# Kernel tuning notes

Measured on AMD Instinct MI355X. Metric: run time of the kernel, lower is better.

## Reference

```python
import jax, jax.numpy as jnp
import numpy as np

B, S, D = 2, 2048, 1024
H = 16
HD = D // H


def setup_inputs() -> dict:
    key = jax.random.key(0)
    k = jax.random.split(key, 5)
    s = 0.02
    return {
        "x": jax.random.normal(k[0], (B, S, D), jnp.float32),
        "w_qkv": jax.random.normal(k[1], (3 * D, D), jnp.float32) * s,
        "b_qkv": jax.random.normal(k[2], (3 * D,), jnp.float32) * s,
        "w_out": jax.random.normal(k[3], (D, D), jnp.float32) * s,
        "b_out": jax.random.normal(k[4], (D,), jnp.float32) * s,
    }


def reference(x, w_qkv, b_qkv, w_out, b_out):
    b, s, d = x.shape
    h, hd = H, HD
    scale = hd ** -0.5
    # QKV projection: [B,S,3D] -> [3,B,H,S,hd]
    qkv = x @ w_qkv.T + b_qkv
    qkv = qkv.reshape(b, s, 3, h, hd).transpose(2, 0, 3, 1, 4)
    q, k, v = qkv[0], qkv[1], qkv[2]
    # Attention scores [B,H,S,S]
    scores = jnp.einsum("bhqd,bhkd->bhqk", q, k) * scale
    attn = jax.nn.softmax(scores, axis=-1)
    # Attend and merge heads
    attended = jnp.einsum("bhqk,bhkd->bqhd", attn, v).reshape(b, s, d)
    return attended @ w_out.T + b_out
```

## Files before the change

kernel.cpp:

```cpp
#include <hip/hip_runtime.h>
#include <hip/hip_bf16.h>

typedef __hip_bfloat16 bf16;
typedef __attribute__((ext_vector_type(8))) short short8;
typedef __attribute__((ext_vector_type(8))) __bf16 bf16x8;
typedef __attribute__((ext_vector_type(4))) float f32x4;
typedef __attribute__((ext_vector_type(16))) float f32x16;
typedef __attribute__((ext_vector_type(4))) unsigned int u32x4;
typedef __attribute__((ext_vector_type(2))) unsigned int u32x2;

#define MFMA16(a, b, c)                                                        \
  __builtin_amdgcn_mfma_f32_16x16x32_bf16(__builtin_bit_cast(bf16x8, (a)),     \
                                          __builtin_bit_cast(bf16x8, (b)),     \
                                          (c), 0, 0, 0)
#define MFMA32(a, b, c)                                                        \
  __builtin_amdgcn_mfma_f32_32x32x16_bf16(__builtin_bit_cast(bf16x8, (a)),     \
                                          __builtin_bit_cast(bf16x8, (b)),     \
                                          (c), 0, 0, 0)

#define GLD16(gsrc, ldst)                                                      \
  __builtin_amdgcn_global_load_lds(                                            \
      (const __attribute__((address_space(1))) void*)(gsrc),                   \
      (__attribute__((address_space(3))) void*)(ldst), 16, 0, 0)

__device__ inline short f2bfs(float f) {
  return __builtin_bit_cast(short, __float2bfloat16(f));
}
__device__ inline unsigned pk2(float lo, float hi) {
  unsigned a = (unsigned short)__builtin_bit_cast(short, __float2bfloat16(lo));
  unsigned b = (unsigned short)__builtin_bit_cast(short, __float2bfloat16(hi));
  return a | (b << 16);
}

template <typename T> __device__ inline short8 ld8bf(const T* p);
template <> __device__ inline short8 ld8bf<bf16>(const bf16* p) {
  return *(const short8*)p;
}
template <> __device__ inline short8 ld8bf<float>(const float* p) {
  f32x4 a = *(const f32x4*)p;
  f32x4 b = *(const f32x4*)(p + 4);
  short8 r;
  r[0] = f2bfs(a[0]); r[1] = f2bfs(a[1]); r[2] = f2bfs(a[2]); r[3] = f2bfs(a[3]);
  r[4] = f2bfs(b[0]); r[5] = f2bfs(b[1]); r[6] = f2bfs(b[2]); r[7] = f2bfs(b[3]);
  return r;
}

template <typename OT> __device__ inline void st1(OT* p, float v);
template <> __device__ inline void st1<bf16>(bf16* p, float v) {
  *p = __float2bfloat16(v);
}
template <> __device__ inline void st1<float>(float* p, float v) { *p = v; }

__device__ inline unsigned int funnel16(unsigned int hi, unsigned int lo) {
  return (unsigned int)(((((unsigned long long)hi) << 32) | lo) >> 16);
}
__device__ inline short8 rotl8(short8 v, int r) {
  u32x4 W = __builtin_bit_cast(u32x4, v);
  u32x4 T, U, F;
  int wr = r >> 1;
  T[0] = (wr & 1) ? W[1] : W[0];
  T[1] = (wr & 1) ? W[2] : W[1];
  T[2] = (wr & 1) ? W[3] : W[2];
  T[3] = (wr & 1) ? W[0] : W[3];
  U[0] = (wr & 2) ? T[2] : T[0];
  U[1] = (wr & 2) ? T[3] : T[1];
  U[2] = (wr & 2) ? T[0] : T[2];
  U[3] = (wr & 2) ? T[1] : T[3];
  F[0] = (r & 1) ? funnel16(U[1], U[0]) : U[0];
  F[1] = (r & 1) ? funnel16(U[2], U[1]) : U[1];
  F[2] = (r & 1) ? funnel16(U[3], U[2]) : U[2];
  F[3] = (r & 1) ? funnel16(U[0], U[3]) : U[3];
  return __builtin_bit_cast(short8, F);
}

__global__ __launch_bounds__(256) void cvt3(
    const float* __restrict__ s0, bf16* __restrict__ d0, int n0,
    const float* __restrict__ s1, bf16* __restrict__ d1, int n1,
    const float* __restrict__ s2, bf16* __restrict__ d2, int n2) {
  int i = (blockIdx.x * 256 + threadIdx.x) * 8;
  if (i < n0) {
    *(short8*)&d0[i] = ld8bf(s0 + i);
  } else if ((i -= n0) < n1) {
    *(short8*)&d1[i] = ld8bf(s1 + i);
  } else if ((i -= n1) < n2) {
    *(short8*)&d2[i] = ld8bf(s2 + i);
  }
}

template <typename OT>
__global__ __launch_bounds__(256, 2) void gemm_lds_bias(
    const bf16* __restrict__ A, const bf16* __restrict__ B,
    const float* __restrict__ bias, OT* __restrict__ C, int M, int N, int K) {
  __shared__ bf16 As[128][64];
  __shared__ bf16 Bs[128][64];

  const int tid = threadIdx.x;
  const int w = tid >> 6, l = tid & 63;
  const int wr = w >> 1, wc = w & 1;
  const int m0 = blockIdx.y * 128, n0 = blockIdx.x * 128;

  f32x4 acc[4][4] = {};

  const int srow = l >> 3;
  const int scol = (l & 7) * 8;

  for (int kt = 0; kt < K; kt += 64) {
#pragma unroll
    for (int j = 0; j < 4; ++j) {
      int chunk = w * 4 + j;
      int row = chunk * 8 + srow;
      GLD16(A + (size_t)(m0 + row) * K + kt + scol, &As[0][0] + chunk * 512);
      GLD16(B + (size_t)(n0 + row) * K + kt + scol, &Bs[0][0] + chunk * 512);
    }
    __syncthreads();

#pragma unroll
    for (int kk = 0; kk < 2; ++kk) {
      short8 af[4], bfv[4];
#pragma unroll
      for (int i = 0; i < 4; ++i) {
        af[i]  = *(const short8*)&As[wr * 64 + i * 16 + (l & 15)]
                                   [kk * 32 + (l >> 4) * 8];
        bfv[i] = *(const short8*)&Bs[wc * 64 + i * 16 + (l & 15)]
                                   [kk * 32 + (l >> 4) * 8];
      }
#pragma unroll
      for (int i = 0; i < 4; ++i)
#pragma unroll
        for (int jn = 0; jn < 4; ++jn)
          acc[i][jn] = MFMA16(af[i], bfv[jn], acc[i][jn]);
    }
    __syncthreads();
  }

#pragma unroll
  for (int i = 0; i < 4; ++i) {
    int rbase = m0 + wr * 64 + i * 16 + (l >> 4) * 4;
#pragma unroll
    for (int jn = 0; jn < 4; ++jn) {
      int col = n0 + wc * 64 + jn * 16 + (l & 15);
      float bv = bias[col];
#pragma unroll
      for (int r = 0; r < 4; ++r)
        st1(&C[(size_t)(rbase + r) * N + col], acc[i][jn][r] + bv);
    }
  }
}

template <typename AT, typename OT>
__global__ __launch_bounds__(256, 2) void gemm_bt_bias(
    const AT* __restrict__ A, const float* __restrict__ B,
    const float* __restrict__ bias, OT* __restrict__ C, int M, int N, int K) {
  __shared__ bf16 As[128][64];
  __shared__ bf16 Bs[128][64];

  const int tid = threadIdx.x;
  const int w = tid >> 6, l = tid & 63;
  const int wr = w >> 1, wc = w & 1;
  const int m0 = blockIdx.y * 128, n0 = blockIdx.x * 128;

  f32x4 acc[4][4] = {};

  const int srow = tid >> 3;
  const int scol = (tid & 7) * 8;

  for (int kt = 0; kt < K; kt += 64) {
    short8 aReg[4], bReg[4];
#pragma unroll
    for (int p = 0; p < 4; ++p) {
      int row = p * 32 + srow;
      aReg[p] = ld8bf(A + (size_t)(m0 + row) * K + kt + scol);
      bReg[p] = ld8bf(B + (size_t)(n0 + row) * K + kt + scol);
    }
    __syncthreads();
#pragma unroll
    for (int p = 0; p < 4; ++p) {
      int row = p * 32 + srow;
      *(short8*)&As[row][scol] = aReg[p];
      *(short8*)&Bs[row][scol] = bReg[p];
    }
    __syncthreads();

#pragma unroll
    for (int kk = 0; kk < 2; ++kk) {
      short8 af[4], bfv[4];
#pragma unroll
      for (int i = 0; i < 4; ++i) {
        af[i]  = *(const short8*)&As[wr * 64 + i * 16 + (l & 15)]
                                   [kk * 32 + (l >> 4) * 8];
        bfv[i] = *(const short8*)&Bs[wc * 64 + i * 16 + (l & 15)]
                                   [kk * 32 + (l >> 4) * 8];
      }
#pragma unroll
      for (int i = 0; i < 4; ++i)
#pragma unroll
        for (int jn = 0; jn < 4; ++jn)
          acc[i][jn] = MFMA16(af[i], bfv[jn], acc[i][jn]);
    }
  }

#pragma unroll
  for (int i = 0; i < 4; ++i) {
    int rbase = m0 + wr * 64 + i * 16 + (l >> 4) * 4;
#pragma unroll
    for (int jn = 0; jn < 4; ++jn) {
      int col = n0 + wc * 64 + jn * 16 + (l & 15);
      float bv = bias[col];
#pragma unroll
      for (int r = 0; r < 4; ++r)
        st1(&C[(size_t)(rbase + r) * N + col], acc[i][jn][r] + bv);
    }
  }
}

__global__ __launch_bounds__(256, 2) void attn_fwd(
    const bf16* __restrict__ qkv, bf16* __restrict__ attended) {
  const int S = 2048, D3 = 3072, D = 1024;
  const int flat = blockIdx.y * 16 + blockIdx.x;
  const int n = (flat & 7) * 64 + (flat >> 3);
  const int qt = n & 15, bh = n >> 4;
  const int b = bh >> 4, h = bh & 15;
  const int tid = threadIdx.x, w = tid >> 6, l = tid & 63;
  const int lo5 = l & 31, hi = l >> 5;

  __shared__ bf16 Klds[128][72];
  __shared__ bf16 Vt[64][136];

  const int q0w = qt * 128 + w * 32;

  short8 qf[4];
  {
    size_t qrow = (size_t)(b * S + q0w + lo5) * D3 + h * 64;
#pragma unroll
    for (int ks = 0; ks < 4; ++ks)
      qf[ks] = *(const short8*)&qkv[qrow + ks * 16 + hi * 8];
  }

  float m_raw = -1e30f, l_i = 0.f;
  f32x16 o0 = {}, o1 = {};

  const float Cs = 0.125f * 1.44269504088896340736f;

  const int srow = tid >> 2;
  const int scq = tid & 3;
  const size_t gb0 = (size_t)(b * S + srow) * D3 + h * 64 + scq * 16;
  const size_t HSTEP = (size_t)64 * D3;

  short8 k0, k1, k2, k3, v0, v1, v2, v3;
  {
    const bf16* g = qkv + gb0;
    k0 = *(const short8*)&g[1024];
    k1 = *(const short8*)&g[1024 + 8];
    v0 = *(const short8*)&g[2048];
    v1 = *(const short8*)&g[2048 + 8];
    const bf16* g2 = g + HSTEP;
    k2 = *(const short8*)&g2[1024];
    k3 = *(const short8*)&g2[1024 + 8];
    v2 = *(const short8*)&g2[2048];
    v3 = *(const short8*)&g2[2048 + 8];
  }

#define PACKP(G, SV)                                                           \
  {                                                                            \
    _Pragma("unroll") for (int tq = 0; tq < 4; ++tq) {                         \
      po[G][tq][0] = pk2((SV)[4 * tq], (SV)[4 * tq + 1]);                      \
      po[G][tq][1] = pk2((SV)[4 * tq + 2], (SV)[4 * tq + 3]);                  \
    }                                                                          \
  }

  for (int t = 0; t < 16; ++t) {
    __syncthreads();
    *(short8*)&Klds[srow][scq * 16] = k0;
    *(short8*)&Klds[srow][scq * 16 + 8] = k1;
    *(short8*)&Klds[64 + srow][scq * 16] = k2;
    *(short8*)&Klds[64 + srow][scq * 16 + 8] = k3;
#pragma unroll
    for (int g = 0; g < 2; ++g) {
      int sI = scq * 2 + g;
      short8 ua = rotl8(g ? v1 : v0, sI);
      short8 ub = rotl8(g ? v3 : v2, sI);
#pragma unroll
      for (int j = 0; j < 8; ++j) {
        int jj = (j + sI) & 7;
        *(short*)&Vt[sI * 8 + jj][srow] = (short)ua[j];
        *(short*)&Vt[sI * 8 + jj][64 + srow] = (short)ub[j];
      }
    }
    __syncthreads();

    if (t + 1 < 16) {
      const bf16* g = qkv + gb0 + (size_t)(t + 1) * 2 * HSTEP;
      k0 = *(const short8*)&g[1024];
      k1 = *(const short8*)&g[1024 + 8];
      k2 = *(const short8*)&g[HSTEP + 1024];
      k3 = *(const short8*)&g[HSTEP + 1024 + 8];
    }

    f32x16 s0 = {}, s1 = {}, s2 = {}, s3 = {};
    __builtin_amdgcn_s_setprio(1);
#pragma unroll
    for (int ks = 0; ks < 4; ++ks) {
      short8 km0 = *(const short8*)&Klds[lo5][ks * 16 + hi * 8];
      short8 km1 = *(const short8*)&Klds[32 + lo5][ks * 16 + hi * 8];
      short8 km2 = *(const short8*)&Klds[64 + lo5][ks * 16 + hi * 8];
      short8 km3 = *(const short8*)&Klds[96 + lo5][ks * 16 + hi * 8];
      s0 = MFMA32(km0, qf[ks], s0);
      s1 = MFMA32(km1, qf[ks], s1);
      s2 = MFMA32(km2, qf[ks], s2);
      s3 = MFMA32(km3, qf[ks], s3);
    }
    __builtin_amdgcn_s_setprio(0);

    if (t + 1 < 16) {
      const bf16* g = qkv + gb0 + (size_t)(t + 1) * 2 * HSTEP;
      v0 = *(const short8*)&g[2048];
      v1 = *(const short8*)&g[2048 + 8];
      v2 = *(const short8*)&g[HSTEP + 2048];
      v3 = *(const short8*)&g[HSTEP + 2048 + 8];
    }

    f32x16 tm;
#pragma unroll
    for (int r = 0; r < 16; ++r)
      tm[r] = fmaxf(fmaxf(s0[r], s1[r]), fmaxf(s2[r], s3[r]));
#pragma unroll
    for (int st = 8; st > 0; st >>= 1)
#pragma unroll
      for (int r = 0; r < st; ++r) tm[r] = fmaxf(tm[r], tm[r + st]);
    float mx = fmaxf(tm[0], __shfl_xor(tm[0], 32));

    bool deferred = __all((mx - m_raw) * Cs <= 8.0f);
    float mn, alpha;
    if (deferred) {
      mn = m_raw;
      alpha = 1.0f;
    } else {
      mn = fmaxf(m_raw, mx);
      alpha = __builtin_amdgcn_exp2f((m_raw - mn) * Cs);
      m_raw = mn;
    }
    float pc = mn * Cs;

#pragma unroll
    for (int r = 0; r < 16; ++r) {
      s0[r] = __builtin_amdgcn_exp2f(__builtin_fmaf(s0[r], Cs, -pc));
      s1[r] = __builtin_amdgcn_exp2f(__builtin_fmaf(s1[r], Cs, -pc));
      s2[r] = __builtin_amdgcn_exp2f(__builtin_fmaf(s2[r], Cs, -pc));
      s3[r] = __builtin_amdgcn_exp2f(__builtin_fmaf(s3[r], Cs, -pc));
    }
    f32x16 ts;
#pragma unroll
    for (int r = 0; r < 16; ++r)
      ts[r] = (s0[r] + s1[r]) + (s2[r] + s3[r]);
#pragma unroll
    for (int st = 8; st > 0; st >>= 1)
#pragma unroll
      for (int r = 0; r < st; ++r) ts[r] += ts[r + st];
    float sf = ts[0] + __shfl_xor(ts[0], 32);
    if (deferred) {
      l_i += sf;
    } else {
      l_i = l_i * alpha + sf;
      o0 *= alpha;
      o1 *= alpha;
    }

    unsigned po[4][4][2];
    PACKP(0, s0) PACKP(1, s1) PACKP(2, s2) PACKP(3, s3)
    unsigned pr[4][2][2];
#pragma unroll
    for (int g = 0; g < 4; ++g)
#pragma unroll
      for (int p = 0; p < 2; ++p)
#pragma unroll
        for (int hf = 0; hf < 2; ++hf) {
          unsigned y = hi ? po[g][2 * p][hf] : po[g][2 * p + 1][hf];
          pr[g][p][hf] = (unsigned)__shfl_xor((int)y, 32);
        }

    __builtin_amdgcn_s_setprio(1);
#pragma unroll
    for (int ks2 = 0; ks2 < 8; ++ks2) {
      const int g = ks2 >> 1, p = ks2 & 1;
      u32x4 fw;
      fw[0] = hi ? pr[g][p][0] : po[g][2 * p][0];
      fw[1] = hi ? pr[g][p][1] : po[g][2 * p][1];
      fw[2] = hi ? po[g][2 * p + 1][0] : pr[g][p][0];
      fw[3] = hi ? po[g][2 * p + 1][1] : pr[g][p][1];
      short8 pf = __builtin_bit_cast(short8, fw);
      short8 va0 = *(const short8*)&Vt[lo5][ks2 * 16 + hi * 8];
      short8 va1 = *(const short8*)&Vt[32 + lo5][ks2 * 16 + hi * 8];
      o0 = MFMA32(va0, pf, o0);
      o1 = MFMA32(va1, pf, o1);
    }
    __builtin_amdgcn_s_setprio(0);
  }

  float inv = 1.0f / l_i;
  size_t orow = (size_t)(b * S + q0w + lo5) * D + h * 64;
#pragma unroll
  for (int t = 0; t < 4; ++t) {
    u32x2 w0, w1;
    w0[0] = pk2(o0[4 * t] * inv, o0[4 * t + 1] * inv);
    w0[1] = pk2(o0[4 * t + 2] * inv, o0[4 * t + 3] * inv);
    w1[0] = pk2(o1[4 * t] * inv, o1[4 * t + 1] * inv);
    w1[1] = pk2(o1[4 * t + 2] * inv, o1[4 * t + 3] * inv);
    *(u32x2*)&attended[orow + 8 * t + 4 * hi] = w0;
    *(u32x2*)&attended[orow + 32 + 8 * t + 4 * hi] = w1;
  }
}

extern "C" void kernel_launch(void* const* d_in, const int* in_sizes, int n_in,
                              void* d_out, int out_size, void* d_ws,
                              size_t ws_size, hipStream_t stream) {
  const float* x     = (const float*)d_in[0];
  const float* w_qkv = (const float*)d_in[1];
  const float* b_qkv = (const float*)d_in[2];
  const float* w_out = (const float*)d_in[3];
  const float* b_out = (const float*)d_in[4];
  float* out = (float*)d_out;

  const int BS = 4096;
  const int D = 1024, D3 = 3072;
  const int NX = BS * D, NWQ = D3 * D, NWO = D * D;

  bf16* qkv = (bf16*)d_ws;
  bf16* att = qkv + (size_t)BS * D3;

  const size_t NEED = ((size_t)BS * D3 + (size_t)BS * D + (size_t)D3 * D +
                       (size_t)D * D) * sizeof(bf16);

  if (ws_size >= NEED) {
    bf16* xb  = att;
    bf16* wqb = xb + (size_t)NX;
    bf16* wob = wqb + (size_t)NWQ;

    int ncvt = (NX + NWQ + NWO) / 8;
    cvt3<<<(ncvt + 255) / 256, 256, 0, stream>>>(x, xb, NX, w_qkv, wqb, NWQ,
                                                 w_out, wob, NWO);
    gemm_lds_bias<bf16><<<dim3(D3 / 128, BS / 128), 256, 0, stream>>>(
        xb, wqb, b_qkv, qkv, BS, D3, D);
    attn_fwd<<<dim3(16, 32), 256, 0, stream>>>(qkv, att);
    gemm_lds_bias<float><<<dim3(D / 128, BS / 128), 256, 0, stream>>>(
        att, wob, b_out, out, BS, D, D);
  } else {
    gemm_bt_bias<float, bf16><<<dim3(D3 / 128, BS / 128), 256, 0, stream>>>(
        x, w_qkv, b_qkv, qkv, BS, D3, D);
    attn_fwd<<<dim3(16, 32), 256, 0, stream>>>(qkv, att);
    gemm_bt_bias<bf16, float><<<dim3(D / 128, BS / 128), 256, 0, stream>>>(
        att, w_out, b_out, out, BS, D, D);
  }
}
```

Before: 127.3 us.

## Narrow output GEMM tile, use permlane32_swap for P exchange, flatten max reduction

The output projection GEMM becomes templated on N tile width and is launched with 64-wide tiles, doubling its block count so the 256 CUs are better filled for the small 4096x1024 output. In attention, the two-step shfl_xor exchange of packed P values between half-waves is replaced with the permlane32_swap intrinsic, which swaps rows directly without ds_bpermute traffic. The row-max reduction is also rewritten as a shallower tree of fmax3-friendly operations. Narrower tiles lower per-block reuse of the A operand.

```diff
diff --git a/kernel.cpp b/kernel.cpp
--- a/kernel.cpp
+++ b/kernel.cpp
@@ -87,19 +87,21 @@
   }
 }
 
-template <typename OT>
+template <int BN, typename OT>
 __global__ __launch_bounds__(256, 2) void gemm_lds_bias(
     const bf16* __restrict__ A, const bf16* __restrict__ B,
     const float* __restrict__ bias, OT* __restrict__ C, int M, int N, int K) {
   __shared__ bf16 As[128][64];
-  __shared__ bf16 Bs[128][64];
+  __shared__ bf16 Bs[BN][64];
 
   const int tid = threadIdx.x;
   const int w = tid >> 6, l = tid & 63;
   const int wr = w >> 1, wc = w & 1;
-  const int m0 = blockIdx.y * 128, n0 = blockIdx.x * 128;
-
-  f32x4 acc[4][4] = {};
+  const int m0 = blockIdx.y * 128, n0 = blockIdx.x * BN;
+  const int JN = BN / 64;
+  const int WCOL = BN / 2;
+
+  f32x4 acc[4][2 * JN] = {};
 
   const int srow = l >> 3;
   const int scol = (l & 7) * 8;
@@ -110,24 +112,30 @@
       int chunk = w * 4 + j;
       int row = chunk * 8 + srow;
       GLD16(A + (size_t)(m0 + row) * K + kt + scol, &As[0][0] + chunk * 512);
+    }
+#pragma unroll
+    for (int j = 0; j < BN / 32; ++j) {
+      int chunk = w * (BN / 32) + j;
+      int row = chunk * 8 + srow;
       GLD16(B + (size_t)(n0 + row) * K + kt + scol, &Bs[0][0] + chunk * 512);
     }
     __syncthreads();
 
 #pragma unroll
     for (int kk = 0; kk < 2; ++kk) {
-      short8 af[4], bfv[4];
-#pragma unroll
-      for (int i = 0; i < 4; ++i) {
-        af[i]  = *(const short8*)&As[wr * 64 + i * 16 + (l & 15)]
-                                   [kk * 32 + (l >> 4) * 8];
-        bfv[i] = *(const short8*)&Bs[wc * 64 + i * 16 + (l & 15)]
-                                   [kk * 32 + (l >> 4) * 8];
-      }
+      short8 af[4], bfv[2 * JN];
 #pragma unroll
       for (int i = 0; i < 4; ++i)
-#pragma unroll
-        for (int jn = 0; jn < 4; ++jn)
+        af[i] = *(const short8*)&As[wr * 64 + i * 16 + (l & 15)]
+                                  [kk * 32 + (l >> 4) * 8];
+#pragma unroll
+      for (int jn = 0; jn < 2 * JN; ++jn)
+        bfv[jn] = *(const short8*)&Bs[wc * WCOL + jn * 16 + (l & 15)]
+                                    [kk * 32 + (l >> 4) * 8];
+#pragma unroll
+      for (int i = 0; i < 4; ++i)
+#pragma unroll
+        for (int jn = 0; jn < 2 * JN; ++jn)
           acc[i][jn] = MFMA16(af[i], bfv[jn], acc[i][jn]);
     }
     __syncthreads();
@@ -137,8 +145,8 @@
   for (int i = 0; i < 4; ++i) {
     int rbase = m0 + wr * 64 + i * 16 + (l >> 4) * 4;
 #pragma unroll
-    for (int jn = 0; jn < 4; ++jn) {
-      int col = n0 + wc * 64 + jn * 16 + (l & 15);
+    for (int jn = 0; jn < 2 * JN; ++jn) {
+      int col = n0 + wc * WCOL + jn * 16 + (l & 15);
       float bv = bias[col];
 #pragma unroll
       for (int r = 0; r < 4; ++r)
@@ -322,12 +330,16 @@
     f32x16 tm;
 #pragma unroll
     for (int r = 0; r < 16; ++r)
-      tm[r] = fmaxf(fmaxf(s0[r], s1[r]), fmaxf(s2[r], s3[r]));
-#pragma unroll
-    for (int st = 8; st > 0; st >>= 1)
-#pragma unroll
-      for (int r = 0; r < st; ++r) tm[r] = fmaxf(tm[r], tm[r + st]);
-    float mx = fmaxf(tm[0], __shfl_xor(tm[0], 32));
+      tm[r] = fmaxf(fmaxf(fmaxf(s0[r], s1[r]), s2[r]), s3[r]);
+    float a0 = fmaxf(fmaxf(tm[0], tm[1]), tm[2]);
+    float a1 = fmaxf(fmaxf(tm[3], tm[4]), tm[5]);
+    float a2 = fmaxf(fmaxf(tm[6], tm[7]), tm[8]);
+    float a3 = fmaxf(fmaxf(tm[9], tm[10]), tm[11]);
+    float a4 = fmaxf(fmaxf(tm[12], tm[13]), tm[14]);
+    float b0v = fmaxf(fmaxf(a0, a1), a2);
+    float b1v = fmaxf(fmaxf(a3, a4), tm[15]);
+    float mx = fmaxf(b0v, b1v);
+    mx = fmaxf(mx, __shfl_xor(mx, 32));
 
     bool deferred = __all((mx - m_raw) * Cs <= 8.0f);
     float mn, alpha;
@@ -367,26 +379,22 @@
 
     unsigned po[4][4][2];
     PACKP(0, s0) PACKP(1, s1) PACKP(2, s2) PACKP(3, s3)
-    unsigned pr[4][2][2];
-#pragma unroll
-    for (int g = 0; g < 4; ++g)
-#pragma unroll
-      for (int p = 0; p < 2; ++p)
-#pragma unroll
-        for (int hf = 0; hf < 2; ++hf) {
-          unsigned y = hi ? po[g][2 * p][hf] : po[g][2 * p + 1][hf];
-          pr[g][p][hf] = (unsigned)__shfl_xor((int)y, 32);
-        }
 
     __builtin_amdgcn_s_setprio(1);
 #pragma unroll
     for (int ks2 = 0; ks2 < 8; ++ks2) {
       const int g = ks2 >> 1, p = ks2 & 1;
+      u32x2 ra = __builtin_amdgcn_permlane32_swap(po[g][2 * p][0],
+                                                  po[g][2 * p + 1][0],
+                                                  false, false);
+      u32x2 rb = __builtin_amdgcn_permlane32_swap(po[g][2 * p][1],
+                                                  po[g][2 * p + 1][1],
+                                                  false, false);
       u32x4 fw;
-      fw[0] = hi ? pr[g][p][0] : po[g][2 * p][0];
-      fw[1] = hi ? pr[g][p][1] : po[g][2 * p][1];
-      fw[2] = hi ? po[g][2 * p + 1][0] : pr[g][p][0];
-      fw[3] = hi ? po[g][2 * p + 1][1] : pr[g][p][1];
+      fw[0] = ra[0];
+      fw[1] = rb[0];
+      fw[2] = ra[1];
+      fw[3] = rb[1];
       short8 pf = __builtin_bit_cast(short8, fw);
       short8 va0 = *(const short8*)&Vt[lo5][ks2 * 16 + hi * 8];
       short8 va1 = *(const short8*)&Vt[32 + lo5][ks2 * 16 + hi * 8];
@@ -438,10 +446,10 @@
     int ncvt = (NX + NWQ + NWO) / 8;
     cvt3<<<(ncvt + 255) / 256, 256, 0, stream>>>(x, xb, NX, w_qkv, wqb, NWQ,
                                                  w_out, wob, NWO);
-    gemm_lds_bias<bf16><<<dim3(D3 / 128, BS / 128), 256, 0, stream>>>(
+    gemm_lds_bias<128, bf16><<<dim3(D3 / 128, BS / 128), 256, 0, stream>>>(
         xb, wqb, b_qkv, qkv, BS, D3, D);
     attn_fwd<<<dim3(16, 32), 256, 0, stream>>>(qkv, att);
-    gemm_lds_bias<float><<<dim3(D / 128, BS / 128), 256, 0, stream>>>(
+    gemm_lds_bias<64, float><<<dim3(D / 64, BS / 128), 256, 0, stream>>>(
         att, wob, b_out, out, BS, D, D);
   } else {
     gemm_bt_bias<float, bf16><<<dim3(D3 / 128, BS / 128), 256, 0, stream>>>(
```

After: 122.7 us. 1.04x faster.
